# Kernel optimization log

Measured on AMD Instinct MI355X. Metric: run time of the kernel, lower is better.

Reference implementation:

```python
import jax, jax.numpy as jnp
import numpy as np

IN_FEATURES = 4096
OUT_FEATURES = 12288
INT8_MAX = 127.0


def setup_inputs() -> dict:
    key = jax.random.key(0)
    kx, kw, ks, kb = jax.random.split(key, 4)
    x = jax.random.normal(kx, (8192, IN_FEATURES), dtype=jnp.float32)
    # pre-quantized int8 weight, stored [out_features, in_features] like the torch module
    weight = jax.random.randint(kw, (OUT_FEATURES, IN_FEATURES), -127, 128, dtype=jnp.int8)
    # per-output-channel weight scale, [out_features, 1]
    weight_scale = (jax.random.uniform(ks, (OUT_FEATURES, 1), dtype=jnp.float32) * 0.02 + 1e-4)
    bias = jax.random.normal(kb, (OUT_FEATURES,), dtype=jnp.float32) * 0.01
    return {"x": x, "weight": weight, "weight_scale": weight_scale, "bias": bias}


def _dynamic_int8_quant(x):
    # symmetric per-token quantization: scale = amax(|x|) / 127
    amax = jnp.max(jnp.abs(x), axis=-1, keepdims=True)  # [M, 1]
    scale = jnp.maximum(amax, 1e-8) / INT8_MAX
    x_q = jnp.clip(jnp.round(x / scale), -INT8_MAX, INT8_MAX).astype(jnp.int8)
    return x_q, scale


def reference(x, weight, weight_scale, bias):
    x_q, x_scale = _dynamic_int8_quant(x)                    # [M,K] int8, [M,1] f32
    # int8 GEMM with int32 accumulation: [M,K] @ [K,N]
    acc = jnp.matmul(x_q.astype(jnp.int32), weight.T.astype(jnp.int32))  # [M,N] int32
    # epilogue: dequant with per-token and per-channel scales, then bias add
    out = acc.astype(jnp.float32) * x_scale * weight_scale[:, 0][None, :] + bias[None, :]
    return out.astype(x.dtype)
```

## Files before the change

kernel.cpp:

```cpp
#include <hip/hip_runtime.h>
#include <stdint.h>

#define M_DIM 8192
#define K_DIM 4096
#define N_DIM 12288

typedef int v4i __attribute__((ext_vector_type(4)));

#define GLDS16(g, l)                                                         \
  __builtin_amdgcn_global_load_lds(                                          \
      (const __attribute__((address_space(1))) void*)(g),                    \
      (__attribute__((address_space(3))) void*)(l), 16, 0, 0)

#define BARRIER() asm volatile("s_barrier" ::: "memory")
#define VMCNT0() asm volatile("s_waitcnt vmcnt(0)" ::: "memory")

__global__ __launch_bounds__(256) void prep(const float* __restrict__ x,
                                            int8_t* __restrict__ xq,
                                            float* __restrict__ xs,
                                            const int* __restrict__ w32,
                                            int8_t* __restrict__ w8) {
  const int t = threadIdx.x;
  if ((int)blockIdx.x < M_DIM) {
    const int row = blockIdx.x;
    const float* xr = x + (size_t)row * K_DIM;

    float4 v[4];
    float amax = 0.f;
#pragma unroll
    for (int i = 0; i < 4; ++i) {
      v[i] = reinterpret_cast<const float4*>(xr)[t * 4 + i];
      amax = fmaxf(amax, fmaxf(fmaxf(fabsf(v[i].x), fabsf(v[i].y)),
                               fmaxf(fabsf(v[i].z), fabsf(v[i].w))));
    }
#pragma unroll
    for (int off = 32; off > 0; off >>= 1)
      amax = fmaxf(amax, __shfl_xor(amax, off));

    __shared__ float smax[4];
    if ((t & 63) == 0) smax[t >> 6] = amax;
    __syncthreads();
    amax = fmaxf(fmaxf(smax[0], smax[1]), fmaxf(smax[2], smax[3]));

    const float scale = fmaxf(amax, 1e-8f) / 127.f;

    union {
      int8_t b[16];
      v4i v;
    } p;
    const float* pv = reinterpret_cast<const float*>(v);
#pragma unroll
    for (int i = 0; i < 16; ++i) {
      float r = rintf(pv[i] / scale);
      r = fminf(127.f, fmaxf(-127.f, r));
      p.b[i] = (int8_t)(int)r;
    }
    reinterpret_cast<v4i*>(xq + (size_t)row * K_DIM)[t] = p.v;
    if (t == 0) xs[row] = scale;
  } else {
    const size_t i = (((size_t)blockIdx.x - M_DIM) * 256 + t) * 16;
    const int4* src = reinterpret_cast<const int4*>(w32 + i);
    union {
      int8_t b[16];
      v4i v;
    } p;
#pragma unroll
    for (int c = 0; c < 4; ++c) {
      int4 q = src[c];
      p.b[c * 4 + 0] = (int8_t)q.x;
      p.b[c * 4 + 1] = (int8_t)q.y;
      p.b[c * 4 + 2] = (int8_t)q.z;
      p.b[c * 4 + 3] = (int8_t)q.w;
    }
    *reinterpret_cast<v4i*>(w8 + i) = p.v;
  }
}

#define BM 256
#define BN 256
#define BKB 128
#define NTILES (K_DIM / BKB)

__global__ __launch_bounds__(512, 2) void gemm_i8(
    const int8_t* __restrict__ xq, const float* __restrict__ xs,
    const int8_t* __restrict__ w8, const float* __restrict__ wsc,
    const float* __restrict__ bias, float* __restrict__ out) {
  __shared__ __align__(16) int8_t lds[131072];

  const int t = threadIdx.x;
  const int lane = t & 63;
  const int w = t >> 6;
  const int wr = w >> 2;
  const int wc = w & 3;
  const int fr = lane & 15;
  const int kq = lane >> 4;
  const int l7 = lane & 7;

  const int bid = (int)blockIdx.x;
  const int xcd = bid & 7;
  const int q = bid >> 3;
  const int g = q >> 5;
  const int j = q & 31;
  const int rowBase = (xcd * 4 + (j >> 3)) * BM;
  const int colBase = (g * 8 + (j & 7)) * BN;

  const int srow = t >> 3;
  const int gslot = (t & 7) ^ (srow & 7);
  const int8_t* gA = xq + (size_t)(rowBase + srow) * K_DIM + gslot * 16;
  const int8_t* gB = w8 + (size_t)(colBase + srow) * K_DIM + gslot * 16;
  int8_t* ldsw = lds + w * 1024;

#define STAGE_A(c, r0, k0) \
  GLDS16(gA + (size_t)(r0) * K_DIM + (k0), ldsw + (c) * 32768 + (r0) * 128)
#define STAGE_B(c, r0, k0) \
  GLDS16(gB + (size_t)(r0) * K_DIM + (k0), ldsw + 65536 + (c) * 32768 + (r0) * 128)

#define STAGE8(d, k1)                                                         \
  STAGE_B(d, 0, k1); STAGE_B(d, 64, k1);                                      \
  STAGE_B(d, 128, k1); STAGE_B(d, 192, k1);                                   \
  STAGE_A(d, 0, k1); STAGE_A(d, 64, k1);                                      \
  STAGE_A(d, 128, k1); STAGE_A(d, 192, k1);

  const int s0_ = kq ^ l7;
  const int s1_ = s0_ ^ 4;
  const int rA = wr * 128 + fr;
  const int rB = wc * 64 + fr;

  const v4i* pA0 = (const v4i*)lds + ((rA << 3) + s0_);
  const v4i* pA1 = (const v4i*)lds + ((rA << 3) + s1_);
  const v4i* pB0 = (const v4i*)(lds + 65536) + ((rB << 3) + s0_);
  const v4i* pB1 = (const v4i*)(lds + 65536) + ((rB << 3) + s1_);

#define LDA(dst, c, mh, ks)                                                   \
  {                                                                           \
    const v4i* _p = (ks) ? pA1 : pA0;                                         \
    dst[0] = _p[((c) << 11) + (((mh) * 64 + 0) << 3)];                        \
    dst[1] = _p[((c) << 11) + (((mh) * 64 + 16) << 3)];                       \
    dst[2] = _p[((c) << 11) + (((mh) * 64 + 32) << 3)];                       \
    dst[3] = _p[((c) << 11) + (((mh) * 64 + 48) << 3)];                       \
  }
#define LDB(dst, c, ks)                                                       \
  {                                                                           \
    const v4i* _p = (ks) ? pB1 : pB0;                                         \
    dst[0] = _p[((c) << 11) + (0 << 3)];                                      \
    dst[1] = _p[((c) << 11) + (16 << 3)];                                     \
    dst[2] = _p[((c) << 11) + (32 << 3)];                                     \
    dst[3] = _p[((c) << 11) + (48 << 3)];                                     \
  }

#define MFMA_BLK(MH, A_, B_)                                                  \
  __builtin_amdgcn_s_setprio(1);                                              \
  _Pragma("unroll") for (int ni = 0; ni < 4; ++ni)                            \
      _Pragma("unroll") for (int mi = 0; mi < 4; ++mi)                        \
          acc[(MH) * 4 + mi][ni] = __builtin_amdgcn_mfma_i32_16x16x64_i8(     \
              A_[mi], B_[ni], acc[(MH) * 4 + mi][ni], 0, 0, 0);               \
  __builtin_amdgcn_s_setprio(0);

  v4i acc[8][4];
#pragma unroll
  for (int i = 0; i < 8; ++i)
#pragma unroll
    for (int jj = 0; jj < 4; ++jj) acc[i][jj] = (v4i){0, 0, 0, 0};

  v4i a0[4], a1[4], b0[4], b1[4];

#define TILE(c, d, k1)                                                        \
  STAGE8(d, k1);                                                              \
  LDA(a1, c, 1, 0);                                                           \
  MFMA_BLK(0, a0, b0);                                                        \
  LDA(a0, c, 0, 1);                                                           \
  LDB(b1, c, 1);                                                              \
  MFMA_BLK(1, a1, b0);                                                        \
  LDA(a1, c, 1, 1);                                                           \
  MFMA_BLK(0, a0, b1);                                                        \
  MFMA_BLK(1, a1, b1);                                                        \
  VMCNT0();                                                                   \
  BARRIER();                                                                  \
  LDA(a0, d, 0, 0);                                                           \
  LDB(b0, d, 0);

#define TILE_LAST(c)                                                          \
  LDA(a1, c, 1, 0);                                                           \
  MFMA_BLK(0, a0, b0);                                                        \
  LDA(a0, c, 0, 1);                                                           \
  LDB(b1, c, 1);                                                              \
  MFMA_BLK(1, a1, b0);                                                        \
  LDA(a1, c, 1, 1);                                                           \
  MFMA_BLK(0, a0, b1);                                                        \
  MFMA_BLK(1, a1, b1);

  STAGE8(0, 0);
  VMCNT0();
  BARRIER();
  LDA(a0, 0, 0, 0);
  LDB(b0, 0, 0);

  for (int tt = 0; tt < NTILES - 2; tt += 2) {
    TILE(0, 1, (tt + 1) * BKB);
    TILE(1, 0, (tt + 2) * BKB);
  }
  TILE(0, 1, (NTILES - 1) * BKB);
  TILE_LAST(1);

  const int orow0 = rowBase + wr * 128;
  const int ocol0 = colBase + wc * 64;
  const int rsub = kq * 4;
#pragma unroll
  for (int mi8 = 0; mi8 < 8; ++mi8) {
    const int r0 = orow0 + mi8 * 16 + rsub;
    const float4 s4v = *reinterpret_cast<const float4*>(xs + r0);
    const float s4[4] = {s4v.x, s4v.y, s4v.z, s4v.w};
#pragma unroll
    for (int ni = 0; ni < 4; ++ni) {
      const int col = ocol0 + ni * 16 + fr;
      const float wf = wsc[col];
      const float bb = bias[col];
#pragma unroll
      for (int r = 0; r < 4; ++r)
        out[(size_t)(r0 + r) * N_DIM + col] =
            (float)acc[mi8][ni][r] * s4[r] * wf + bb;
    }
  }
}

extern "C" void kernel_launch(void* const* d_in, const int* in_sizes, int n_in,
                              void* d_out, int out_size, void* d_ws,
                              size_t ws_size, hipStream_t stream) {
  const float* x = (const float*)d_in[0];
  const int* w32 = (const int*)d_in[1];
  const float* wscale = (const float*)d_in[2];
  const float* bias = (const float*)d_in[3];
  float* out = (float*)d_out;

  int8_t* xq = (int8_t*)d_ws;
  float* xs = (float*)((char*)d_ws + (size_t)M_DIM * K_DIM);
  int8_t* w8 = (int8_t*)((char*)d_ws + (size_t)M_DIM * K_DIM + M_DIM * 4);

  const int packBlocks = (N_DIM * K_DIM) / (256 * 16);
  prep<<<M_DIM + packBlocks, 256, 0, stream>>>(x, xq, xs, w32, w8);
  gemm_i8<<<(M_DIM / BM) * (N_DIM / BN), 512, 0, stream>>>(xq, xs, w8, wscale,
                                                           bias, out);
}
```

Baseline: 461.2 us.

## Shrink GEMM tile to 128x256 with 64-byte K step and four waves

Reworks the int8 GEMM tiling: block tile drops from 256x256 to 128x256, the K step from 128 to 64 bytes, and the block from 8 to 4 waves, each wave computing 128x64. LDS drops from 128KB to 48KB, and the swizzle, staging and fragment-load layout are rewritten to match. The aim is more resident blocks per CU and less LDS pressure. In exchange each loaded byte is reused less, there are twice as many barrier/tile iterations, and the grid doubles.

After: 532.4 us. 15.4% more time.

```diff
diff --git a/kernel.cpp b/kernel.cpp
--- a/kernel.cpp
+++ b/kernel.cpp
@@ -76,76 +76,66 @@
   }
 }
 
-#define BM 256
+#define BM 128
 #define BN 256
-#define BKB 128
+#define BKB 64
 #define NTILES (K_DIM / BKB)
 
-__global__ __launch_bounds__(512, 2) void gemm_i8(
+__global__ __launch_bounds__(256, 2) void gemm_i8(
     const int8_t* __restrict__ xq, const float* __restrict__ xs,
     const int8_t* __restrict__ w8, const float* __restrict__ wsc,
     const float* __restrict__ bias, float* __restrict__ out) {
-  __shared__ __align__(16) int8_t lds[131072];
+  __shared__ __align__(16) int8_t lds[49152];
 
   const int t = threadIdx.x;
   const int lane = t & 63;
   const int w = t >> 6;
-  const int wr = w >> 2;
-  const int wc = w & 3;
   const int fr = lane & 15;
   const int kq = lane >> 4;
-  const int l7 = lane & 7;
 
   const int bid = (int)blockIdx.x;
   const int xcd = bid & 7;
   const int q = bid >> 3;
   const int g = q >> 5;
   const int j = q & 31;
-  const int rowBase = (xcd * 4 + (j >> 3)) * BM;
-  const int colBase = (g * 8 + (j & 7)) * BN;
-
-  const int srow = t >> 3;
-  const int gslot = (t & 7) ^ (srow & 7);
+  const int rowBase = (xcd * 8 + (j >> 2)) * BM;
+  const int colBase = (g * 4 + (j & 3)) * BN;
+
+  const int srow = t >> 2;
+  const int gslot = (t & 3) ^ ((srow >> 1) & 3);
   const int8_t* gA = xq + (size_t)(rowBase + srow) * K_DIM + gslot * 16;
   const int8_t* gB = w8 + (size_t)(colBase + srow) * K_DIM + gslot * 16;
   int8_t* ldsw = lds + w * 1024;
 
 #define STAGE_A(c, r0, k0) \
-  GLDS16(gA + (size_t)(r0) * K_DIM + (k0), ldsw + (c) * 32768 + (r0) * 128)
+  GLDS16(gA + (size_t)(r0) * K_DIM + (k0), ldsw + (c) * 8192 + (r0) * 64)
 #define STAGE_B(c, r0, k0) \
-  GLDS16(gB + (size_t)(r0) * K_DIM + (k0), ldsw + 65536 + (c) * 32768 + (r0) * 128)
-
-#define STAGE8(d, k1)                                                         \
+  GLDS16(gB + (size_t)(r0) * K_DIM + (k0), ldsw + 16384 + (c) * 16384 + (r0) * 64)
+
+#define STAGE6(d, k1)                                                         \
   STAGE_B(d, 0, k1); STAGE_B(d, 64, k1);                                      \
   STAGE_B(d, 128, k1); STAGE_B(d, 192, k1);                                   \
-  STAGE_A(d, 0, k1); STAGE_A(d, 64, k1);                                      \
-  STAGE_A(d, 128, k1); STAGE_A(d, 192, k1);
-
-  const int s0_ = kq ^ l7;
-  const int s1_ = s0_ ^ 4;
-  const int rA = wr * 128 + fr;
-  const int rB = wc * 64 + fr;
-
-  const v4i* pA0 = (const v4i*)lds + ((rA << 3) + s0_);
-  const v4i* pA1 = (const v4i*)lds + ((rA << 3) + s1_);
-  const v4i* pB0 = (const v4i*)(lds + 65536) + ((rB << 3) + s0_);
-  const v4i* pB1 = (const v4i*)(lds + 65536) + ((rB << 3) + s1_);
-
-#define LDA(dst, c, mh, ks)                                                   \
+  STAGE_A(d, 0, k1); STAGE_A(d, 64, k1);
+
+  const int sA = kq ^ ((fr >> 1) & 3);
+
+  const v4i* pA = (const v4i*)lds + (fr * 4 + sA);
+  const v4i* pB = (const v4i*)(lds + 16384) + ((w * 64 + fr) * 4 + sA);
+
+#define LDA_LO(dst, c)                                                        \
   {                                                                           \
-    const v4i* _p = (ks) ? pA1 : pA0;                                         \
-    dst[0] = _p[((c) << 11) + (((mh) * 64 + 0) << 3)];                        \
-    dst[1] = _p[((c) << 11) + (((mh) * 64 + 16) << 3)];                       \
-    dst[2] = _p[((c) << 11) + (((mh) * 64 + 32) << 3)];                       \
-    dst[3] = _p[((c) << 11) + (((mh) * 64 + 48) << 3)];                       \
-  }
-#define LDB(dst, c, ks)                                                       \
+    _Pragma("unroll") for (int mi = 0; mi < 4; ++mi)                          \
+        dst[mi] = pA[((c) << 9) + (mi << 6)];                                 \
+  }
+#define LDA_HI(dst, c)                                                        \
   {                                                                           \
-    const v4i* _p = (ks) ? pB1 : pB0;                                         \
-    dst[0] = _p[((c) << 11) + (0 << 3)];                                      \
-    dst[1] = _p[((c) << 11) + (16 << 3)];                                     \
-    dst[2] = _p[((c) << 11) + (32 << 3)];                                     \
-    dst[3] = _p[((c) << 11) + (48 << 3)];                                     \
+    _Pragma("unroll") for (int mi = 0; mi < 4; ++mi)                          \
+        dst[mi] = pA[((c) << 9) + ((mi + 4) << 6)];                           \
+  }
+#define LDB4(dst, c)                                                          \
+  {                                                                           \
+    _Pragma("unroll") for (int ni = 0; ni < 4; ++ni)                          \
+        dst[ni] = pB[((c) << 10) + (ni << 6)];                                \
   }
 
 #define MFMA_BLK(MH, A_, B_)                                                  \
@@ -162,38 +152,28 @@
 #pragma unroll
     for (int jj = 0; jj < 4; ++jj) acc[i][jj] = (v4i){0, 0, 0, 0};
 
-  v4i a0[4], a1[4], b0[4], b1[4];
+  v4i a0[4], a1[4], b0[4];
 
 #define TILE(c, d, k1)                                                        \
-  STAGE8(d, k1);                                                              \
-  LDA(a1, c, 1, 0);                                                           \
+  STAGE6(d, k1);                                                              \
+  LDA_HI(a1, c);                                                              \
   MFMA_BLK(0, a0, b0);                                                        \
-  LDA(a0, c, 0, 1);                                                           \
-  LDB(b1, c, 1);                                                              \
   MFMA_BLK(1, a1, b0);                                                        \
-  LDA(a1, c, 1, 1);                                                           \
-  MFMA_BLK(0, a0, b1);                                                        \
-  MFMA_BLK(1, a1, b1);                                                        \
   VMCNT0();                                                                   \
   BARRIER();                                                                  \
-  LDA(a0, d, 0, 0);                                                           \
-  LDB(b0, d, 0);
+  LDA_LO(a0, d);                                                              \
+  LDB4(b0, d);
 
 #define TILE_LAST(c)                                                          \
-  LDA(a1, c, 1, 0);                                                           \
+  LDA_HI(a1, c);                                                              \
   MFMA_BLK(0, a0, b0);                                                        \
-  LDA(a0, c, 0, 1);                                                           \
-  LDB(b1, c, 1);                                                              \
-  MFMA_BLK(1, a1, b0);                                                        \
-  LDA(a1, c, 1, 1);                                                           \
-  MFMA_BLK(0, a0, b1);                                                        \
-  MFMA_BLK(1, a1, b1);
-
-  STAGE8(0, 0);
+  MFMA_BLK(1, a1, b0);
+
+  STAGE6(0, 0);
   VMCNT0();
   BARRIER();
-  LDA(a0, 0, 0, 0);
-  LDB(b0, 0, 0);
+  LDA_LO(a0, 0);
+  LDB4(b0, 0);
 
   for (int tt = 0; tt < NTILES - 2; tt += 2) {
     TILE(0, 1, (tt + 1) * BKB);
@@ -202,12 +182,12 @@
   TILE(0, 1, (NTILES - 1) * BKB);
   TILE_LAST(1);
 
-  const int orow0 = rowBase + wr * 128;
-  const int ocol0 = colBase + wc * 64;
+  const int orow0 = rowBase;
+  const int ocol0 = colBase + w * 64;
   const int rsub = kq * 4;
 #pragma unroll
-  for (int mi8 = 0; mi8 < 8; ++mi8) {
-    const int r0 = orow0 + mi8 * 16 + rsub;
+  for (int mi = 0; mi < 8; ++mi) {
+    const int r0 = orow0 + mi * 16 + rsub;
     const float4 s4v = *reinterpret_cast<const float4*>(xs + r0);
     const float s4[4] = {s4v.x, s4v.y, s4v.z, s4v.w};
 #pragma unroll
@@ -218,7 +198,7 @@
 #pragma unroll
       for (int r = 0; r < 4; ++r)
         out[(size_t)(r0 + r) * N_DIM + col] =
-            (float)acc[mi8][ni][r] * s4[r] * wf + bb;
+            (float)acc[mi][ni][r] * s4[r] * wf + bb;
     }
   }
 }
@@ -238,6 +218,6 @@
 
   const int packBlocks = (N_DIM * K_DIM) / (256 * 16);
   prep<<<M_DIM + packBlocks, 256, 0, stream>>>(x, xq, xs, w32, w8);
-  gemm_i8<<<(M_DIM / BM) * (N_DIM / BN), 512, 0, stream>>>(xq, xs, w8, wscale,
+  gemm_i8<<<(M_DIM / BM) * (N_DIM / BN), 256, 0, stream>>>(xq, xs, w8, wscale,
                                                            bias, out);
 }
```
